# Kernel tuning notes

Measured on AMD Instinct MI355X. Metric: run time of the kernel, lower is better.

## Reference

```python
import jax, jax.numpy as jnp
import numpy as np

N_NODES = 100000
N_EDGES = 1600000
D_FEAT = 128
HIDDEN = 128
N_LAYERS = 3
N_GRAPHS = 512
N_CLASSES = 10


def setup_inputs() -> dict:
    key = jax.random.key(0)
    ks = jax.random.split(key, 10)
    x = jax.random.normal(ks[0], (N_NODES, D_FEAT), dtype=jnp.float32)
    edge_index = jax.random.randint(ks[1], (2, N_EDGES), 0, N_NODES, dtype=jnp.int64)
    batch = jnp.sort(jax.random.randint(ks[2], (N_NODES,), 0, N_GRAPHS, dtype=jnp.int64))
    s = 0.05
    W0 = jax.random.normal(ks[3], (D_FEAT, HIDDEN), dtype=jnp.float32) * s
    b0 = jnp.zeros((HIDDEN,), dtype=jnp.float32)
    Ws = jax.random.normal(ks[4], (N_LAYERS, HIDDEN, HIDDEN), dtype=jnp.float32) * s
    bs = jnp.zeros((N_LAYERS, HIDDEN), dtype=jnp.float32)
    linW = jax.random.normal(ks[5], (HIDDEN, N_CLASSES), dtype=jnp.float32) * s
    linb = jnp.zeros((N_CLASSES,), dtype=jnp.float32)
    return {"x": x, "edge_index": edge_index, "batch": batch,
            "W0": W0, "b0": b0, "Ws": Ws, "bs": bs, "linW": linW, "linb": linb}


def _gcn_norm(edge_index, n_nodes):
    # PyG GCNConv default: add self-loops, symmetric D^{-1/2}(A+I)D^{-1/2} normalization
    src, dst = edge_index[0], edge_index[1]
    ones = jnp.ones((edge_index.shape[1],), dtype=jnp.float32)
    deg = jax.ops.segment_sum(ones, dst, num_segments=n_nodes) + 1.0  # +1 for self-loop
    dis = jax.lax.rsqrt(deg)
    edge_coef = (dis[src] * dis[dst])[:, None]   # [E,1]
    self_coef = (dis * dis)[:, None]             # [N,1]
    return src, dst, edge_coef, self_coef


def _gcn_conv(h, W, b, src, dst, edge_coef, self_coef, n_nodes):
    hw = h @ W                                                        # [N,H]
    agg = jax.ops.segment_sum(hw[src] * edge_coef, dst, num_segments=n_nodes)
    return agg + self_coef * hw + b


def reference(x, edge_index, batch, W0, b0, Ws, bs, linW, linb):
    n = N_NODES
    src, dst, ec, sc = _gcn_norm(edge_index, n)
    x_cur = jax.nn.relu(_gcn_conv(x, W0, b0, src, dst, ec, sc, n))
    x_pre = jnp.zeros_like(x_cur)
    for i in range(N_LAYERS):
        x_temp = x_cur
        x_cur = jax.nn.relu(_gcn_conv(x_cur + x_pre, Ws[i], bs[i], src, dst, ec, sc, n))
        x_pre = x_temp
    # global mean pool over graph ids
    sums = jax.ops.segment_sum(x_cur, batch, num_segments=N_GRAPHS)
    cnts = jax.ops.segment_sum(jnp.ones((n,), dtype=x_cur.dtype), batch, num_segments=N_GRAPHS)
    pooled = sums / jnp.maximum(cnts, 1.0)[:, None]
    # dropout is identity in eval mode
    return pooled @ linW + linb
```

## Files before the change

kernel.cpp:

```cpp
#include <hip/hip_runtime.h>

#define NN 100000
#define NE 1600000
#define H  128
#define NG 512
#define NC 10
#define NBUCK  98
#define CHUNK  4096
#define BINCAP 18432
#define EDCAP  22528

typedef _Float16 f16;
typedef __attribute__((ext_vector_type(8))) _Float16 f16x8;
typedef __attribute__((ext_vector_type(4))) _Float16 f16x4;
typedef __attribute__((ext_vector_type(4))) float    f32x4;

__device__ __forceinline__ int lower_bound_i(const int* __restrict__ a, int n, int val) {
    int lo = 0, hi = n;
    while (lo < hi) {
        int mid = (lo + hi) >> 1;
        if (a[mid] < val) lo = mid + 1; else hi = mid;
    }
    return lo;
}

__global__ __launch_bounds__(256) void binA_kernel(const int* __restrict__ src,
                                                   const int* __restrict__ dst,
                                                   int* __restrict__ bcur,
                                                   int* __restrict__ binned) {
    __shared__ int hist[NBUCK];
    __shared__ int lbase[NBUCK];
    __shared__ int gbase[NBUCK];
    __shared__ int cur[NBUCK];
    __shared__ int stage[CHUNK];
    __shared__ int destp[CHUNK];
    int t  = threadIdx.x;
    int e0 = blockIdx.x * CHUNK;
    int cnt = NE - e0; if (cnt > CHUNK) cnt = CHUNK;

    if (t < NBUCK) hist[t] = 0;
    __syncthreads();

    int s_[16], d_[16];
    #pragma unroll
    for (int i = 0; i < 16; ++i) {
        int e = e0 + i * 256 + t;
        if (e < NE) {
            s_[i] = src[e]; d_[i] = dst[e];
            atomicAdd(&hist[d_[i] >> 10], 1);
        } else { s_[i] = -1; d_[i] = 0; }
    }
    __syncthreads();

    if (t < NBUCK) {
        int lb = 0;
        for (int i = 0; i < t; ++i) lb += hist[i];
        lbase[t] = lb;
        cur[t]   = lb;
        gbase[t] = t * BINCAP + atomicAdd(&bcur[t], hist[t]);
    }
    __syncthreads();

    #pragma unroll
    for (int i = 0; i < 16; ++i) {
        if (s_[i] >= 0) {
            int s = s_[i], d = d_[i];
            int b = d >> 10;
            int r = atomicAdd(&cur[b], 1);
            stage[r] = s | ((d & 1023) << 17);
            destp[r] = gbase[b] + (r - lbase[b]);
        }
    }
    __syncthreads();

    #pragma unroll
    for (int i = 0; i < 16; ++i) {
        int idx = i * 256 + t;
        if (idx < cnt) binned[destp[idx]] = stage[idx];
    }
}

__global__ __launch_bounds__(1024) void binB_kernel(const int* __restrict__ binned,
                                                    const int* __restrict__ bcnt,
                                                    int* __restrict__ edata,
                                                    int* __restrict__ offs_pk,
                                                    float* __restrict__ dis) {
    __shared__ int cnt[1024];
    __shared__ int cursor[1024];
    __shared__ int ws[16];
    int b = blockIdx.x, t = threadIdx.x;
    int lane = t & 63, wid = t >> 6;
    cnt[t] = 0;
    __syncthreads();
    int lo = b * BINCAP, hi = lo + bcnt[b];
    for (int e = lo + t; e < hi; e += 1024) {
        atomicAdd(&cnt[(binned[e] >> 17) & 1023], 1);
    }
    __syncthreads();
    int gd = (b << 10) + t;
    int c = cnt[t];
    int L = (gd < NN) ? ((c + 4) & ~3) : 0;
    int incl = L;
    #pragma unroll
    for (int d = 1; d < 64; d <<= 1) { int u = __shfl_up(incl, d, 64); if (lane >= d) incl += u; }
    if (lane == 63) ws[wid] = incl;
    __syncthreads();
    int wbase = 0;
    for (int w = 0; w < wid; ++w) wbase += ws[w];
    int lbase = wbase + incl - L;
    int epoff = b * EDCAP;
    int gbase = epoff + lbase;
    if (gd < NN) {
        offs_pk[gd] = gbase | ((L >> 2) << 22);
        dis[gd] = rsqrtf((float)c + 1.0f);
        edata[gbase] = gd;
        for (int i = c + 1; i < L; ++i) edata[gbase + i] = NN;
    }
    cursor[t] = lbase + 1;
    __syncthreads();
    for (int e = lo + t; e < hi; e += 1024) {
        int p = binned[e];
        int dloc = (p >> 17) & 1023;
        int r = atomicAdd(&cursor[dloc], 1);
        edata[epoff + r] = p & 0x1FFFF;
    }
}

__global__ __launch_bounds__(256) void wprep_kernel(const float* __restrict__ W0,
                                                    const float* __restrict__ Ws,
                                                    f16* __restrict__ wt_hi,
                                                    f16* __restrict__ wt_lo) {
    int idx = blockIdx.x * 256 + threadIdx.x;
    int m = idx >> 14;
    int k = (idx >> 7) & 127;
    int n = idx & 127;
    const float* Wm = (m == 0) ? W0 : (Ws + (size_t)(m - 1) * H * H);
    float v = Wm[k * H + n];
    f16 hi = (f16)v;
    float lo = v - (float)hi;
    wt_hi[(size_t)m * H * H + n * H + k] = hi;
    wt_lo[(size_t)m * H * H + n * H + k] = (f16)lo;
}

template <int FP32IN>
__global__ __launch_bounds__(512) void gemm_kernel(const void* __restrict__ in0,
                                                   const f16* __restrict__ in1,
                                                   const f16* __restrict__ wt_hi,
                                                   const f16* __restrict__ wt_lo,
                                                   const float* __restrict__ dis,
                                                   f16* __restrict__ hw) {
    __shared__ f16x8 sW[2][128 * 16];
    int t = threadIdx.x;
    int l = t & 63, w = t >> 6;
    int lr = l & 15, lq = l >> 4;
    int rowb = blockIdx.x * 256 + w * 32;

    const f16x8* wh = (const f16x8*)wt_hi;
    const f16x8* wl = (const f16x8*)wt_lo;
    #pragma unroll
    for (int i = 0; i < 4; ++i) {
        int ch = i * 512 + t;
        int n = ch >> 4, c = ch & 15;
        int sw = n * 16 + (c ^ (n & 7));
        sW[0][sw] = wh[ch];
        sW[1][sw] = wl[ch];
    }

    f16x8 aF[2][4];
    #pragma unroll
    for (int rt = 0; rt < 2; ++rt) {
        int grow = rowb + rt * 16 + lr;
        if (grow >= NN) grow = NN - 1;
        #pragma unroll
        for (int ks = 0; ks < 4; ++ks) {
            int c = ks * 4 + lq;
            f16x8 v;
            if (FP32IN) {
                const float* xp = (const float*)in0 + (size_t)grow * H + c * 8;
                f32x4 u0 = *(const f32x4*)xp;
                f32x4 u1 = *(const f32x4*)(xp + 4);
                #pragma unroll
                for (int u = 0; u < 4; ++u) { v[u] = (f16)u0[u]; v[u + 4] = (f16)u1[u]; }
            } else {
                v = *((const f16x8*)in0 + (size_t)grow * 16 + c);
                if (in1) {
                    f16x8 uu = *((const f16x8*)in1 + (size_t)grow * 16 + c);
                    v = v + uu;
                }
            }
            aF[rt][ks] = v;
        }
    }
    __syncthreads();

    f32x4 acc[2][8];
    #pragma unroll
    for (int rt = 0; rt < 2; ++rt)
        #pragma unroll
        for (int ct = 0; ct < 8; ++ct)
            acc[rt][ct] = (f32x4){0.f, 0.f, 0.f, 0.f};

    #pragma unroll
    for (int p = 0; p < 2; ++p) {
        #pragma unroll
        for (int ks = 0; ks < 4; ++ks) {
            int c = ks * 4 + lq;
            #pragma unroll
            for (int ct = 0; ct < 8; ++ct) {
                int n = ct * 16 + lr;
                f16x8 bF = sW[p][n * 16 + (c ^ (n & 7))];
                acc[0][ct] = __builtin_amdgcn_mfma_f32_16x16x32_f16(bF, aF[0][ks], acc[0][ct], 0, 0, 0);
                acc[1][ct] = __builtin_amdgcn_mfma_f32_16x16x32_f16(bF, aF[1][ks], acc[1][ct], 0, 0, 0);
            }
        }
    }

    #pragma unroll
    for (int rt = 0; rt < 2; ++rt) {
        int grow = rowb + rt * 16 + lr;
        if (grow < NN) {
            float dv = dis[grow];
            #pragma unroll
            for (int ct = 0; ct < 8; ++ct) {
                f16x4 o;
                #pragma unroll
                for (int r = 0; r < 4; ++r) o[r] = (f16)(dv * acc[rt][ct][r]);
                *(f16x4*)&hw[(size_t)grow * H + ct * 16 + lq * 4] = o;
            }
        }
    }
}

__global__ __launch_bounds__(256) void agg_kernel(const f16* __restrict__ hw,
                                                  const float* __restrict__ dis,
                                                  const int* __restrict__ offs_pk,
                                                  const int* __restrict__ edata,
                                                  const float* __restrict__ bias,
                                                  f16* __restrict__ outh) {
    int wid  = threadIdx.x >> 6;
    int lane = threadIdx.x & 63;
    int node = blockIdx.x * 4 + wid;
    if (node >= NN) return;
    int q  = lane >> 4;
    int j8 = (lane & 15) * 8;
    int w = offs_pk[node];
    int beg = w & 0x3FFFFF;
    int nit4 = (unsigned)w >> 22;
    int nit8 = nit4 >> 1;
    float acc[8];
    #pragma unroll
    for (int u = 0; u < 8; ++u) acc[u] = 0.f;

    for (int it = 0; it < nit8; ++it) {
        int base = beg + it * 8;
        int sa = edata[base + q];
        int sb = edata[base + 4 + q];
        f16x8 va = *(const f16x8*)&hw[(size_t)sa * H + j8];
        f16x8 vb = *(const f16x8*)&hw[(size_t)sb * H + j8];
        f16x8 vs = va + vb;
        #pragma unroll
        for (int u = 0; u < 8; ++u) acc[u] += (float)vs[u];
    }
    if (nit4 & 1) {
        int base = beg + nit8 * 8;
        int sa = edata[base + q];
        f16x8 va = *(const f16x8*)&hw[(size_t)sa * H + j8];
        #pragma unroll
        for (int u = 0; u < 8; ++u) acc[u] += (float)va[u];
    }
    #pragma unroll
    for (int u = 0; u < 8; ++u) {
        acc[u] += __shfl_xor(acc[u], 16, 64);
        acc[u] += __shfl_xor(acc[u], 32, 64);
    }
    if (q == 0) {
        float dv = dis[node];
        f16x8 o;
        #pragma unroll
        for (int u = 0; u < 8; ++u) o[u] = (f16)fmaxf(dv * acc[u] + bias[j8 + u], 0.f);
        *(f16x8*)&outh[(size_t)node * H + j8] = o;
    }
}

__global__ __launch_bounds__(512) void pool_kernel(const f16* __restrict__ h,
                                                   const int* __restrict__ batch,
                                                   const float* __restrict__ linW,
                                                   const float* __restrict__ linb,
                                                   float* __restrict__ out) {
    __shared__ float pld[4][H];
    int g = blockIdx.x;
    int t = threadIdx.x;
    int f = t & 127, quad = t >> 7;
    int lo = lower_bound_i(batch, NN, g);
    int hi = lower_bound_i(batch, NN, g + 1);
    float sum = 0.f;
    for (int n = lo + quad; n < hi; n += 4) sum += (float)h[(size_t)n * H + f];
    pld[quad][f] = sum;
    __syncthreads();
    if (t < H) {
        float cnt = (float)(hi - lo);
        pld[0][t] = (pld[0][t] + pld[1][t] + pld[2][t] + pld[3][t]) / fmaxf(cnt, 1.0f);
    }
    __syncthreads();
    if (t < NC) {
        float acc = linb[t];
        #pragma unroll 4
        for (int j = 0; j < H; ++j) acc += pld[0][j] * linW[j * NC + t];
        out[g * NC + t] = acc;
    }
}

extern "C" void kernel_launch(void* const* d_in, const int* in_sizes, int n_in,
                              void* d_out, int out_size, void* d_ws, size_t ws_size,
                              hipStream_t stream) {
    const float* x     = (const float*)d_in[0];
    const int*   ei    = (const int*)d_in[1];
    const int*   batch = (const int*)d_in[2];
    const float* W0    = (const float*)d_in[3];
    const float* b0    = (const float*)d_in[4];
    const float* Ws    = (const float*)d_in[5];
    const float* bs    = (const float*)d_in[6];
    const float* linW  = (const float*)d_in[7];
    const float* linb  = (const float*)d_in[8];
    const int* src = ei;
    const int* dst = ei + NE;

    char* p = (char*)d_ws;
    auto alloc = [&](size_t bytes) -> void* {
        void* r = (void*)p;
        p += (bytes + 255) & ~(size_t)255;
        return r;
    };
    f16*   buf0    = (f16*)alloc((size_t)NN * H * 2);
    f16*   buf1    = (f16*)alloc((size_t)NN * H * 2);
    f16*   buf2    = (f16*)alloc((size_t)NN * H * 2);
    f16*   hwb     = (f16*)alloc((size_t)(NN + 1) * H * 2);
    f16*   wt_hi   = (f16*)alloc((size_t)4 * H * H * 2);
    f16*   wt_lo   = (f16*)alloc((size_t)4 * H * H * 2);
    float* dis     = (float*)alloc((size_t)NN * 4);
    int*   offs_pk = (int*)alloc((size_t)NN * 4);
    int*   binned  = (int*)alloc((size_t)NBUCK * BINCAP * 4);
    int*   edata   = (int*)alloc((size_t)NBUCK * EDCAP * 4);
    int*   bcur    = (int*)alloc((size_t)NBUCK * 4);

    hipMemsetAsync(bcur, 0, (size_t)NBUCK * 4, stream);
    hipMemsetAsync(hwb + (size_t)NN * H, 0, (size_t)H * 2, stream);

    wprep_kernel<<<(4 * H * H) / 256, 256, 0, stream>>>(W0, Ws, wt_hi, wt_lo);
    binA_kernel<<<(NE + CHUNK - 1) / CHUNK, 256, 0, stream>>>(src, dst, bcur, binned);
    binB_kernel<<<NBUCK, 1024, 0, stream>>>(binned, bcur, edata, offs_pk, dis);

    int gemm_grid = (NN + 255) / 256;
    int agg_grid  = (NN + 3) / 4;
    size_t WSZ = (size_t)H * H;

    gemm_kernel<1><<<gemm_grid, 512, 0, stream>>>(x, nullptr, wt_hi, wt_lo, dis, hwb);
    agg_kernel<<<agg_grid, 256, 0, stream>>>(hwb, dis, offs_pk, edata, b0, buf0);
    gemm_kernel<0><<<gemm_grid, 512, 0, stream>>>(buf0, nullptr, wt_hi + WSZ, wt_lo + WSZ, dis, hwb);
    agg_kernel<<<agg_grid, 256, 0, stream>>>(hwb, dis, offs_pk, edata, bs, buf1);
    gemm_kernel<0><<<gemm_grid, 512, 0, stream>>>(buf1, buf0, wt_hi + 2 * WSZ, wt_lo + 2 * WSZ, dis, hwb);
    agg_kernel<<<agg_grid, 256, 0, stream>>>(hwb, dis, offs_pk, edata, bs + H, buf2);
    gemm_kernel<0><<<gemm_grid, 512, 0, stream>>>(buf2, buf1, wt_hi + 3 * WSZ, wt_lo + 3 * WSZ, dis, hwb);
    agg_kernel<<<agg_grid, 256, 0, stream>>>(hwb, dis, offs_pk, edata, bs + 2 * H, buf0);

    pool_kernel<<<NG, 512, 0, stream>>>(buf0, batch, linW, linb, (float*)d_out);
}
```

Measured before the change: 409.6 us.

## Pad edge lists to multiples of 8 and fold memsets into wprep kernel

Each node's CSR edge list is now padded to a multiple of 8 instead of 4, so the aggregation loop can issue four independent gathers per iteration and keep more memory loads in flight. The bucket capacity is enlarged to hold the extra padding. The two memset calls are removed and their zeroing is done inside the weight-prep kernel, saving launch overhead. The cost is more padding gathers of the zero row, plus a larger edata buffer.

```diff
diff --git a/kernel.cpp b/kernel.cpp
--- a/kernel.cpp
+++ b/kernel.cpp
@@ -8,7 +8,7 @@
 #define NBUCK  98
 #define CHUNK  4096
 #define BINCAP 18432
-#define EDCAP  22528
+#define EDCAP  26624
 
 typedef _Float16 f16;
 typedef __attribute__((ext_vector_type(8))) _Float16 f16x8;
@@ -22,6 +22,29 @@
         if (a[mid] < val) lo = mid + 1; else hi = mid;
     }
     return lo;
+}
+
+__global__ __launch_bounds__(256) void wprep_kernel(const float* __restrict__ W0,
+                                                    const float* __restrict__ Ws,
+                                                    f16* __restrict__ wt_hi,
+                                                    f16* __restrict__ wt_lo,
+                                                    int* __restrict__ bcur,
+                                                    f16* __restrict__ hwb) {
+    int t = threadIdx.x;
+    if (blockIdx.x == 0) {
+        if (t < NBUCK) bcur[t] = 0;
+        if (t >= 128 && t < 192) ((int*)(hwb + (size_t)NN * H))[t - 128] = 0;
+    }
+    int idx = blockIdx.x * 256 + t;
+    int m = idx >> 14;
+    int k = (idx >> 7) & 127;
+    int n = idx & 127;
+    const float* Wm = (m == 0) ? W0 : (Ws + (size_t)(m - 1) * H * H);
+    float v = Wm[k * H + n];
+    f16 hi = (f16)v;
+    float lo = v - (float)hi;
+    wt_hi[(size_t)m * H * H + n * H + k] = hi;
+    wt_lo[(size_t)m * H * H + n * H + k] = (f16)lo;
 }
 
 __global__ __launch_bounds__(256) void binA_kernel(const int* __restrict__ src,
@@ -99,7 +122,7 @@
     __syncthreads();
     int gd = (b << 10) + t;
     int c = cnt[t];
-    int L = (gd < NN) ? ((c + 4) & ~3) : 0;
+    int L = (gd < NN) ? ((c + 8) & ~7) : 0;
     int incl = L;
     #pragma unroll
     for (int d = 1; d < 64; d <<= 1) { int u = __shfl_up(incl, d, 64); if (lane >= d) incl += u; }
@@ -111,7 +134,7 @@
     int epoff = b * EDCAP;
     int gbase = epoff + lbase;
     if (gd < NN) {
-        offs_pk[gd] = gbase | ((L >> 2) << 22);
+        offs_pk[gd] = gbase | ((L >> 3) << 22);
         dis[gd] = rsqrtf((float)c + 1.0f);
         edata[gbase] = gd;
         for (int i = c + 1; i < L; ++i) edata[gbase + i] = NN;
@@ -124,22 +147,6 @@
         int r = atomicAdd(&cursor[dloc], 1);
         edata[epoff + r] = p & 0x1FFFF;
     }
-}
-
-__global__ __launch_bounds__(256) void wprep_kernel(const float* __restrict__ W0,
-                                                    const float* __restrict__ Ws,
-                                                    f16* __restrict__ wt_hi,
-                                                    f16* __restrict__ wt_lo) {
-    int idx = blockIdx.x * 256 + threadIdx.x;
-    int m = idx >> 14;
-    int k = (idx >> 7) & 127;
-    int n = idx & 127;
-    const float* Wm = (m == 0) ? W0 : (Ws + (size_t)(m - 1) * H * H);
-    float v = Wm[k * H + n];
-    f16 hi = (f16)v;
-    float lo = v - (float)hi;
-    wt_hi[(size_t)m * H * H + n * H + k] = hi;
-    wt_lo[(size_t)m * H * H + n * H + k] = (f16)lo;
 }
 
 template <int FP32IN>
@@ -245,28 +252,35 @@
     int j8 = (lane & 15) * 8;
     int w = offs_pk[node];
     int beg = w & 0x3FFFFF;
-    int nit4 = (unsigned)w >> 22;
-    int nit8 = nit4 >> 1;
+    int nit8 = (unsigned)w >> 22;
     float acc[8];
     #pragma unroll
     for (int u = 0; u < 8; ++u) acc[u] = 0.f;
 
-    for (int it = 0; it < nit8; ++it) {
+    int it = 0;
+    for (; it + 2 <= nit8; it += 2) {
         int base = beg + it * 8;
-        int sa = edata[base + q];
-        int sb = edata[base + 4 + q];
-        f16x8 va = *(const f16x8*)&hw[(size_t)sa * H + j8];
-        f16x8 vb = *(const f16x8*)&hw[(size_t)sb * H + j8];
-        f16x8 vs = va + vb;
-        #pragma unroll
-        for (int u = 0; u < 8; ++u) acc[u] += (float)vs[u];
-    }
-    if (nit4 & 1) {
-        int base = beg + nit8 * 8;
-        int sa = edata[base + q];
-        f16x8 va = *(const f16x8*)&hw[(size_t)sa * H + j8];
-        #pragma unroll
-        for (int u = 0; u < 8; ++u) acc[u] += (float)va[u];
+        int s0 = edata[base + q];
+        int s1 = edata[base + 4 + q];
+        int s2 = edata[base + 8 + q];
+        int s3 = edata[base + 12 + q];
+        f16x8 v0 = *(const f16x8*)&hw[(size_t)s0 * H + j8];
+        f16x8 v1 = *(const f16x8*)&hw[(size_t)s1 * H + j8];
+        f16x8 v2 = *(const f16x8*)&hw[(size_t)s2 * H + j8];
+        f16x8 v3 = *(const f16x8*)&hw[(size_t)s3 * H + j8];
+        f16x8 vt = (v0 + v1) + (v2 + v3);
+        #pragma unroll
+        for (int u = 0; u < 8; ++u) acc[u] += (float)vt[u];
+    }
+    if (it < nit8) {
+        int base = beg + it * 8;
+        int s0 = edata[base + q];
+        int s1 = edata[base + 4 + q];
+        f16x8 v0 = *(const f16x8*)&hw[(size_t)s0 * H + j8];
+        f16x8 v1 = *(const f16x8*)&hw[(size_t)s1 * H + j8];
+        f16x8 vt = v0 + v1;
+        #pragma unroll
+        for (int u = 0; u < 8; ++u) acc[u] += (float)vt[u];
     }
     #pragma unroll
     for (int u = 0; u < 8; ++u) {
@@ -343,10 +357,7 @@
     int*   edata   = (int*)alloc((size_t)NBUCK * EDCAP * 4);
     int*   bcur    = (int*)alloc((size_t)NBUCK * 4);
 
-    hipMemsetAsync(bcur, 0, (size_t)NBUCK * 4, stream);
-    hipMemsetAsync(hwb + (size_t)NN * H, 0, (size_t)H * 2, stream);
-
-    wprep_kernel<<<(4 * H * H) / 256, 256, 0, stream>>>(W0, Ws, wt_hi, wt_lo);
+    wprep_kernel<<<(4 * H * H) / 256, 256, 0, stream>>>(W0, Ws, wt_hi, wt_lo, bcur, hwb);
     binA_kernel<<<(NE + CHUNK - 1) / CHUNK, 256, 0, stream>>>(src, dst, bcur, binned);
     binB_kernel<<<NBUCK, 1024, 0, stream>>>(binned, bcur, edata, offs_pk, dis);
 
```

Measured after the change: 396.8 us. 3.1% less time.
